# Optimization experiments

Hardware: AMD Instinct MI355X
Metric: run time of the kernel (lower is better)

Reference implementation:

```python
import jax, jax.numpy as jnp
import numpy as np

T, N = 64, 2048          # timesteps, population
DT = 1e-3                # simulation step
TAU_MEM_INV = 100.0      # LIF membrane 1/tau
V_TH, V_LEAK, V_RESET = 1.0, 0.0, 0.0
TAU_PRE_INV, TAU_POST_INV = 50.0, 50.0   # STDP trace 1/tau
A_PRE, A_POST = 1.0, 1.0                 # trace contributions
ETA_PLUS, ETA_MINUS = 1e-3, 1e-3         # learning rates
W_MIN, W_MAX = 0.0, 1.0                  # hard bounds
ALPHA = 100.0                            # SuperSpike surrogate sharpness

@jax.custom_vjp
def spike(v):
    # Heaviside forward, SuperSpike surrogate backward (as in norse LIF cells)
    return (v > 0.0).astype(v.dtype)

def _spike_fwd(v):
    return spike(v), v

def _spike_bwd(v, g):
    return (g / (ALPHA * jnp.abs(v) + 1.0) ** 2,)

spike.defvjp(_spike_fwd, _spike_bwd)


def setup_inputs() -> dict:
    key = jax.random.key(0)
    k1, k2 = jax.random.split(key)
    # +1.0 bias ensures nonzero spiking activity so STDP actually fires
    exc_current = jax.random.normal(k1, (T, N), dtype=jnp.float32) + 1.0
    # recurrent weights w[post, pre], small positive init within [W_MIN, W_MAX]
    w = jax.random.uniform(k2, (N, N), dtype=jnp.float32) * 0.02
    t_pre = jnp.zeros((N,), jnp.float32)
    t_post = jnp.zeros((N,), jnp.float32)
    return {"exc_current": exc_current, "w": w, "t_pre": t_pre, "t_post": t_post}


def reference(exc_current, w, t_pre, t_post):
    n = w.shape[0]
    z0 = jnp.zeros((n,), w.dtype)  # Layer reset: cell(zeros(population))
    v0 = jnp.zeros((n,), w.dtype)

    def step(carry, x):
        w_, z, v, tp, tpo = carry
        # recurrent synaptic current: w[post, pre] @ z_pre
        i_syn = w_ @ z
        # LIF membrane update
        v = v + DT * TAU_MEM_INV * ((V_LEAK - v) + i_syn + x)
        z_new = spike(v - V_TH)
        v = v * (1.0 - z_new) + V_RESET * z_new  # reset
        # STDP traces (norse stdp_step_linear: update traces, then dw)
        tp = tp + DT * TAU_PRE_INV * (-tp + A_PRE * z_new)
        tpo = tpo + DT * TAU_POST_INV * (-tpo + A_POST * z_new)
        dw = ETA_PLUS * jnp.outer(z_new, tp) - ETA_MINUS * jnp.outer(tpo, z_new)
        w_ = jnp.clip(w_ + dw, W_MIN, W_MAX)  # additive STDP, hard bounds
        return (w_, z_new, v, tp, tpo), z_new

    _, spikes = jax.lax.scan(step, (w, z0, v0, t_pre, t_post), exc_current)
    return spikes  # [T, N], matches torch.stack([self.step(x) for x in exc_current])
```

## Files before the change

### kernel.cpp

```cpp
#include <hip/hip_runtime.h>

constexpr int   T_STEPS = 64;
constexpr int   NN      = 2048;
constexpr float DT_TAU  = 0.1f;
constexpr float V_TH_C  = 1.0f;
constexpr float TRC     = 0.05f;
constexpr float ETA     = 1e-3f;

constexpr int BLOCKS  = 256;
constexpr int THREADS = 512;
constexpr int ROWS_PER_BLOCK = NN / BLOCKS;
constexpr int CHUNKS = NN / 256;

__global__ __launch_bounds__(THREADS)
void snn_msg_kernel(const float* __restrict__ x,
                    const float* __restrict__ w_in,
                    const float* __restrict__ tpre0,
                    const float* __restrict__ tpost0,
                    unsigned long long* __restrict__ zpub,
                    int stride,
                    float*       __restrict__ out)
{
    const int bid  = blockIdx.x;
    const int tid  = threadIdx.x;
    const int wv   = tid >> 6;
    const int lane = tid & 63;
    const int row  = bid * ROWS_PER_BLOCK + wv;

    __shared__ __align__(16) float z_s[NN];
    __shared__ __align__(16) float tp_s[NN];
    __shared__ __align__(16) float x_s[T_STEPS * ROWS_PER_BLOCK];
    __shared__ unsigned zw_s[BLOCKS];
    __shared__ float tpo_s8[ROWS_PER_BLOCK];
    __shared__ float isyn_s8[ROWS_PER_BLOCK];

    float4 tp4 = ((const float4*)tpre0)[tid];
    ((float4*)tp_s)[tid] = tp4;

    x_s[tid] = x[(size_t)(tid >> 3) * NN + bid * ROWS_PER_BLOCK + (tid & 7)];

    float v_own = 0.0f, tpo_own = 0.0f;
    if (tid < ROWS_PER_BLOCK) {
        tpo_own = tpost0[bid * ROWS_PER_BLOCK + tid];
        isyn_s8[tid] = 0.0f;
    }

    const float4* wrow4 = (const float4*)(w_in + (size_t)row * NN);
    float4 wreg[CHUNKS];
    #pragma unroll
    for (int c = 0; c < CHUNKS; ++c) wreg[c] = wrow4[c * 64 + lane];

    __syncthreads();

    for (int t = 0; t < T_STEPS; ++t) {
        const int par = t & 1;

        if (tid < 64) {
            float z = 0.0f;
            float v = 0.0f;
            if (tid < ROWS_PER_BLOCK) {
                v = v_own;
                v = v + DT_TAU * ((0.0f - v) + isyn_s8[tid]
                                  + x_s[t * ROWS_PER_BLOCK + tid]);
                z = (v - V_TH_C > 0.0f) ? 1.0f : 0.0f;
            }
            unsigned long long bits = __ballot(z > 0.0f) & 0xFFull;
            if (t + 1 < T_STEPS && tid == 0) {
                unsigned long long word =
                    ((unsigned long long)(unsigned)(t + 1) << 32) | bits;
                __hip_atomic_store(&zpub[(size_t)(par * BLOCKS + bid) * stride],
                                   word, __ATOMIC_RELAXED,
                                   __HIP_MEMORY_SCOPE_AGENT);
            }
            if (tid < ROWS_PER_BLOCK) {
                v_own   = v * (1.0f - z);
                tpo_own = tpo_own + TRC * (-tpo_own + z);
                tpo_s8[tid] = tpo_own;
                out[(size_t)t * NN + bid * ROWS_PER_BLOCK + tid] = z;
            }
        }
        if (t == T_STEPS - 1) break;

        if (tid < BLOCKS) {
            const unsigned long long* p =
                &zpub[(size_t)(par * BLOCKS + tid) * stride];
            unsigned long long v =
                __hip_atomic_load(p, __ATOMIC_RELAXED, __HIP_MEMORY_SCOPE_AGENT);
            while ((unsigned)(v >> 32) != (unsigned)(t + 1)) {
                asm volatile("s_sleep 1");
                v = __hip_atomic_load(p, __ATOMIC_RELAXED,
                                      __HIP_MEMORY_SCOPE_AGENT);
            }
            zw_s[tid] = (unsigned)v;
        }
        __syncthreads();

        {
            unsigned wbits = zw_s[tid >> 1];
            int sh = (tid & 1) * 4;
            float4 z4;
            z4.x = ((wbits >> (sh + 0)) & 1u) ? 1.0f : 0.0f;
            z4.y = ((wbits >> (sh + 1)) & 1u) ? 1.0f : 0.0f;
            z4.z = ((wbits >> (sh + 2)) & 1u) ? 1.0f : 0.0f;
            z4.w = ((wbits >> (sh + 3)) & 1u) ? 1.0f : 0.0f;
            ((float4*)z_s)[tid] = z4;
            tp4.x = tp4.x + TRC * (-tp4.x + z4.x);
            tp4.y = tp4.y + TRC * (-tp4.y + z4.y);
            tp4.z = tp4.z + TRC * (-tp4.z + z4.z);
            tp4.w = tp4.w + TRC * (-tp4.w + z4.w);
            ((float4*)tp_s)[tid] = tp4;
        }
        __syncthreads();

        const float zi   = z_s[row];
        const float tpoi = tpo_s8[wv];
        float acc = 0.0f;
        const float4* z4s  = (const float4*)z_s;
        const float4* tp4s = (const float4*)tp_s;
        #pragma unroll
        for (int c = 0; c < CHUNKS; ++c) {
            float4 zj = z4s[c * 64 + lane];
            float4 tj = tp4s[c * 64 + lane];
            float nw;
            nw = wreg[c].x + (ETA * (zi * tj.x) - ETA * (tpoi * zj.x));
            nw = fminf(fmaxf(nw, 0.0f), 1.0f); wreg[c].x = nw; acc += nw * zj.x;
            nw = wreg[c].y + (ETA * (zi * tj.y) - ETA * (tpoi * zj.y));
            nw = fminf(fmaxf(nw, 0.0f), 1.0f); wreg[c].y = nw; acc += nw * zj.y;
            nw = wreg[c].z + (ETA * (zi * tj.z) - ETA * (tpoi * zj.z));
            nw = fminf(fmaxf(nw, 0.0f), 1.0f); wreg[c].z = nw; acc += nw * zj.z;
            nw = wreg[c].w + (ETA * (zi * tj.w) - ETA * (tpoi * zj.w));
            nw = fminf(fmaxf(nw, 0.0f), 1.0f); wreg[c].w = nw; acc += nw * zj.w;
        }
        #pragma unroll
        for (int m = 32; m >= 1; m >>= 1) acc += __shfl_xor(acc, m, 64);
        if (lane == 0) isyn_s8[wv] = acc;
        __syncthreads();
    }
}

extern "C" void kernel_launch(void* const* d_in, const int* in_sizes, int n_in,
                              void* d_out, int out_size, void* d_ws, size_t ws_size,
                              hipStream_t stream) {
    const float* x     = (const float*)d_in[0];
    const float* w_in  = (const float*)d_in[1];
    const float* tpre  = (const float*)d_in[2];
    const float* tpost = (const float*)d_in[3];
    float*       out   = (float*)d_out;

    unsigned long long* zpub = (unsigned long long*)d_ws;

    int stride;
    if      (ws_size >= (size_t)2 * BLOCKS * 16 * sizeof(unsigned long long)) stride = 16;
    else if (ws_size >= (size_t)2 * BLOCKS *  8 * sizeof(unsigned long long)) stride = 8;
    else                                                                      stride = 1;

    void* args[] = {(void*)&x, (void*)&w_in, (void*)&tpre, (void*)&tpost,
                    (void*)&zpub, (void*)&stride, (void*)&out};
    hipLaunchCooperativeKernel((void*)snn_msg_kernel,
                               dim3(BLOCKS), dim3(THREADS),
                               args, 0, stream);
}
```

Before: 282.3 us.

## Replace block barriers with per-wave flags and LDS atomic spike aggregation

Removes all __syncthreads from the time loop. Each wave now computes its own neuron's LIF update redundantly across its lanes and counts in with an LDS fetch-add; the last wave to arrive publishes the block's spike word. All eight waves poll 32 global flags each, then decode and write their own chunk of z and the pre-trace into LDS. A per-chunk release/acquire flag tells other waves when that chunk is ready, replacing the block-wide barriers. This removes serialization through wave 0 and the barrier latency on each step, at the cost of LDS spin-waiting and more subtle ordering that depends on the global barrier to keep buffers from being reused too early.

```diff
diff --git a/kernel.cpp b/kernel.cpp
--- a/kernel.cpp
+++ b/kernel.cpp
@@ -30,111 +30,112 @@
     __shared__ __align__(16) float z_s[NN];
     __shared__ __align__(16) float tp_s[NN];
     __shared__ __align__(16) float x_s[T_STEPS * ROWS_PER_BLOCK];
-    __shared__ unsigned zw_s[BLOCKS];
-    __shared__ float tpo_s8[ROWS_PER_BLOCK];
-    __shared__ float isyn_s8[ROWS_PER_BLOCK];
+    __shared__ int      done_s[CHUNKS];
+    __shared__ unsigned word_s[2];
 
     float4 tp4 = ((const float4*)tpre0)[tid];
-    ((float4*)tp_s)[tid] = tp4;
 
     x_s[tid] = x[(size_t)(tid >> 3) * NN + bid * ROWS_PER_BLOCK + (tid & 7)];
 
-    float v_own = 0.0f, tpo_own = 0.0f;
-    if (tid < ROWS_PER_BLOCK) {
-        tpo_own = tpost0[bid * ROWS_PER_BLOCK + tid];
-        isyn_s8[tid] = 0.0f;
-    }
+    if (tid < CHUNKS) done_s[tid] = 0;
+    if (tid < 2)      word_s[tid] = 0u;
+
+    float v_own   = 0.0f;
+    float tpo_own = tpost0[row];
 
     const float4* wrow4 = (const float4*)(w_in + (size_t)row * NN);
     float4 wreg[CHUNKS];
     #pragma unroll
     for (int c = 0; c < CHUNKS; ++c) wreg[c] = wrow4[c * 64 + lane];
 
+    float isyn = 0.0f;
     __syncthreads();
 
-    for (int t = 0; t < T_STEPS; ++t) {
-        const int par = t & 1;
+    for (int k = 0; k < T_STEPS; ++k) {
+        const int par = k & 1;
 
-        if (tid < 64) {
-            float z = 0.0f;
-            float v = 0.0f;
-            if (tid < ROWS_PER_BLOCK) {
-                v = v_own;
-                v = v + DT_TAU * ((0.0f - v) + isyn_s8[tid]
-                                  + x_s[t * ROWS_PER_BLOCK + tid]);
-                z = (v - V_TH_C > 0.0f) ? 1.0f : 0.0f;
-            }
-            unsigned long long bits = __ballot(z > 0.0f) & 0xFFull;
-            if (t + 1 < T_STEPS && tid == 0) {
-                unsigned long long word =
-                    ((unsigned long long)(unsigned)(t + 1) << 32) | bits;
+        float xk = x_s[k * ROWS_PER_BLOCK + wv];
+        float v  = v_own + DT_TAU * ((0.0f - v_own) + isyn + xk);
+        float z  = (v - V_TH_C > 0.0f) ? 1.0f : 0.0f;
+        v_own    = v * (1.0f - z);
+        tpo_own  = tpo_own + TRC * (-tpo_own + z);
+        if (lane == 0) out[(size_t)k * NN + row] = z;
+        if (k == T_STEPS - 1) break;
+
+        if (lane == 0) {
+            unsigned add = 0x01000000u | (z > 0.0f ? (1u << wv) : 0u);
+            unsigned old = __hip_atomic_fetch_add(&word_s[par], add,
+                               __ATOMIC_RELAXED, __HIP_MEMORY_SCOPE_WORKGROUP);
+            if ((old >> 24) == 7u) {
+                unsigned bits = (old + add) & 0xFFu;
+                __hip_atomic_store(&word_s[par], 0u,
+                                   __ATOMIC_RELAXED, __HIP_MEMORY_SCOPE_WORKGROUP);
+                unsigned long long wrd =
+                    ((unsigned long long)(unsigned)(k + 1) << 32) | bits;
                 __hip_atomic_store(&zpub[(size_t)(par * BLOCKS + bid) * stride],
-                                   word, __ATOMIC_RELAXED,
-                                   __HIP_MEMORY_SCOPE_AGENT);
-            }
-            if (tid < ROWS_PER_BLOCK) {
-                v_own   = v * (1.0f - z);
-                tpo_own = tpo_own + TRC * (-tpo_own + z);
-                tpo_s8[tid] = tpo_own;
-                out[(size_t)t * NN + bid * ROWS_PER_BLOCK + tid] = z;
+                                   wrd, __ATOMIC_RELAXED, __HIP_MEMORY_SCOPE_AGENT);
             }
         }
-        if (t == T_STEPS - 1) break;
 
-        if (tid < BLOCKS) {
+        unsigned my_bits = 0u;
+        if (lane < 32) {
             const unsigned long long* p =
-                &zpub[(size_t)(par * BLOCKS + tid) * stride];
-            unsigned long long v =
-                __hip_atomic_load(p, __ATOMIC_RELAXED, __HIP_MEMORY_SCOPE_AGENT);
-            while ((unsigned)(v >> 32) != (unsigned)(t + 1)) {
-                asm volatile("s_sleep 1");
-                v = __hip_atomic_load(p, __ATOMIC_RELAXED,
-                                      __HIP_MEMORY_SCOPE_AGENT);
+                &zpub[(size_t)(par * BLOCKS + (wv * 32 + lane)) * stride];
+            unsigned long long pv = __hip_atomic_load(p, __ATOMIC_RELAXED,
+                                        __HIP_MEMORY_SCOPE_AGENT);
+            while ((unsigned)(pv >> 32) != (unsigned)(k + 1)) {
+                __builtin_amdgcn_s_sleep(1);
+                pv = __hip_atomic_load(p, __ATOMIC_RELAXED,
+                                       __HIP_MEMORY_SCOPE_AGENT);
             }
-            zw_s[tid] = (unsigned)v;
+            my_bits = (unsigned)pv;
         }
-        __syncthreads();
 
-        {
-            unsigned wbits = zw_s[tid >> 1];
-            int sh = (tid & 1) * 4;
-            float4 z4;
-            z4.x = ((wbits >> (sh + 0)) & 1u) ? 1.0f : 0.0f;
-            z4.y = ((wbits >> (sh + 1)) & 1u) ? 1.0f : 0.0f;
-            z4.z = ((wbits >> (sh + 2)) & 1u) ? 1.0f : 0.0f;
-            z4.w = ((wbits >> (sh + 3)) & 1u) ? 1.0f : 0.0f;
-            ((float4*)z_s)[tid] = z4;
-            tp4.x = tp4.x + TRC * (-tp4.x + z4.x);
-            tp4.y = tp4.y + TRC * (-tp4.y + z4.y);
-            tp4.z = tp4.z + TRC * (-tp4.z + z4.z);
-            tp4.w = tp4.w + TRC * (-tp4.w + z4.w);
-            ((float4*)tp_s)[tid] = tp4;
-        }
-        __syncthreads();
+        unsigned wbits = (unsigned)__shfl((int)my_bits, lane >> 1, 64);
+        int sh = (lane & 1) * 4;
+        float4 z4;
+        z4.x = ((wbits >> (sh + 0)) & 1u) ? 1.0f : 0.0f;
+        z4.y = ((wbits >> (sh + 1)) & 1u) ? 1.0f : 0.0f;
+        z4.z = ((wbits >> (sh + 2)) & 1u) ? 1.0f : 0.0f;
+        z4.w = ((wbits >> (sh + 3)) & 1u) ? 1.0f : 0.0f;
+        tp4.x = tp4.x + TRC * (-tp4.x + z4.x);
+        tp4.y = tp4.y + TRC * (-tp4.y + z4.y);
+        tp4.z = tp4.z + TRC * (-tp4.z + z4.z);
+        tp4.w = tp4.w + TRC * (-tp4.w + z4.w);
 
-        const float zi   = z_s[row];
-        const float tpoi = tpo_s8[wv];
+        ((float4*)z_s)[tid]  = z4;
+        ((float4*)tp_s)[tid] = tp4;
+        if (lane == 0)
+            __hip_atomic_store(&done_s[wv], k + 1,
+                               __ATOMIC_RELEASE, __HIP_MEMORY_SCOPE_WORKGROUP);
+
+        const float zi_own = z;
+        const float tpoi   = tpo_own;
         float acc = 0.0f;
         const float4* z4s  = (const float4*)z_s;
         const float4* tp4s = (const float4*)tp_s;
         #pragma unroll
         for (int c = 0; c < CHUNKS; ++c) {
+            if (c != wv) {
+                while (__hip_atomic_load(&done_s[c], __ATOMIC_ACQUIRE,
+                                         __HIP_MEMORY_SCOPE_WORKGROUP) < k + 1) {}
+            }
             float4 zj = z4s[c * 64 + lane];
             float4 tj = tp4s[c * 64 + lane];
             float nw;
-            nw = wreg[c].x + (ETA * (zi * tj.x) - ETA * (tpoi * zj.x));
+            nw = wreg[c].x + (ETA * (zi_own * tj.x) - ETA * (tpoi * zj.x));
             nw = fminf(fmaxf(nw, 0.0f), 1.0f); wreg[c].x = nw; acc += nw * zj.x;
-            nw = wreg[c].y + (ETA * (zi * tj.y) - ETA * (tpoi * zj.y));
+            nw = wreg[c].y + (ETA * (zi_own * tj.y) - ETA * (tpoi * zj.y));
             nw = fminf(fmaxf(nw, 0.0f), 1.0f); wreg[c].y = nw; acc += nw * zj.y;
-            nw = wreg[c].z + (ETA * (zi * tj.z) - ETA * (tpoi * zj.z));
+            nw = wreg[c].z + (ETA * (zi_own * tj.z) - ETA * (tpoi * zj.z));
             nw = fminf(fmaxf(nw, 0.0f), 1.0f); wreg[c].z = nw; acc += nw * zj.z;
-            nw = wreg[c].w + (ETA * (zi * tj.w) - ETA * (tpoi * zj.w));
+            nw = wreg[c].w + (ETA * (zi_own * tj.w) - ETA * (tpoi * zj.w));
             nw = fminf(fmaxf(nw, 0.0f), 1.0f); wreg[c].w = nw; acc += nw * zj.w;
         }
+
         #pragma unroll
         for (int m = 32; m >= 1; m >>= 1) acc += __shfl_xor(acc, m, 64);
-        if (lane == 0) isyn_s8[wv] = acc;
-        __syncthreads();
+        isyn = acc;
     }
 }
 
```

Result: slower. 309.4 us (+9.6%).
